# Performance work log

Measured on AMD Instinct MI355X. Metric: run time of the kernel, lower is better.

Reference implementation:

```python
import jax, jax.numpy as jnp
import numpy as np

LN_EPS = 1e-5
DEG_EPS = 1e-6
H = 256
N_VAR = 100000
NUM_CON = 50000
E = 300000


def setup_inputs() -> dict:
    key = jax.random.key(0)
    ks = jax.random.split(key, 8)
    s = 1.0 / np.sqrt(H)
    s2 = 1.0 / np.sqrt(H + 1)
    return {
        "x_var": jax.random.normal(ks[0], (N_VAR, H), dtype=jnp.float32),
        "src": jax.random.randint(ks[1], (E,), 0, N_VAR, dtype=jnp.int32),
        "dst": jax.random.randint(ks[2], (E,), 0, NUM_CON, dtype=jnp.int32),
        "clue_values": jax.random.normal(ks[3], (NUM_CON,), dtype=jnp.float32),
        "num_con": NUM_CON,
        "msg_W": jax.random.uniform(ks[4], (H, H), jnp.float32, -s, s),
        "msg_b": jax.random.uniform(ks[5], (H,), jnp.float32, -s, s),
        "update_W": jax.random.uniform(ks[6], (H, H + 1), jnp.float32, -s2, s2),
        "update_b": jax.random.uniform(ks[7], (H,), jnp.float32, -s2, s2),
        "ln_w": jnp.ones((H,), jnp.float32),
        "ln_b": jnp.zeros((H,), jnp.float32),
    }


def reference(x_var, src, dst, clue_values, num_con, msg_W, msg_b, update_W, update_b, ln_w, ln_b):
    # gather + linear message transform: (E, H)
    msgs = x_var[src] @ msg_W.T + msg_b
    # degree-normalized scatter-add into constraints: (num_con, H)
    agg = jax.ops.segment_sum(msgs, dst, num_segments=num_con)
    deg = jax.ops.segment_sum(jnp.ones((dst.shape[0],), msgs.dtype), dst, num_segments=num_con)
    agg = agg / (deg[:, None] + DEG_EPS)
    # concat clue scalar, update MLP, ReLU
    h = jnp.concatenate([agg, clue_values[:, None]], axis=1)
    out = jax.nn.relu(h @ update_W.T + update_b)
    # LayerNorm over last dim
    mu = out.mean(axis=-1, keepdims=True)
    var = out.var(axis=-1, keepdims=True)
    return (out - mu) * jax.lax.rsqrt(var + LN_EPS) * ln_w + ln_b
```

## Files before the change

### kernel.cpp

```cpp
#include <hip/hip_runtime.h>

#define HD 256
#define LN_EPS 1e-5f
#define DEG_EPS 1e-6f
#define CAP 64
#define C2 264

typedef __attribute__((ext_vector_type(8))) short short8;
typedef __attribute__((ext_vector_type(4))) short s16x4;
typedef __attribute__((ext_vector_type(4))) float f32x4;
typedef __attribute__((ext_vector_type(4))) int i32x4;

__device__ inline unsigned short f2bf(float f) {
    union { float f; unsigned int u; } v; v.f = f;
    unsigned int r = v.u + 0x7FFFu + ((v.u >> 16) & 1u);
    return (unsigned short)(r >> 16);
}
__device__ inline float bf2f(unsigned short h) {
    union { unsigned int u; float f; } v; v.u = ((unsigned int)h) << 16;
    return v.f;
}

__global__ __launch_bounds__(256) void prep0_kernel(
    int* __restrict__ counts, int num_con,
    const float* __restrict__ msg_W, const float* __restrict__ msg_b,
    const float* __restrict__ upd_W,
    unsigned short* __restrict__ w12b, float* __restrict__ bv,
    float* __restrict__ ucol, int zb) {
    int b = blockIdx.x, tid = threadIdx.x;
    if (b < zb) {
        int i = (b * 256 + tid) * 4;
        if (i + 4 <= num_con) *(i32x4*)(counts + i) = (i32x4){0, 0, 0, 0};
        else for (; i < num_con; ++i) counts[i] = 0;
    } else {
        int j = b - zb, k = tid;
        float a0 = 0.f, a1 = 0.f, a2 = 0.f, a3 = 0.f, accb = 0.f;
#pragma unroll 2
        for (int m = 0; m < 256; m += 4) {
            float w0 = upd_W[j * 257 + m + 0];
            float w1 = upd_W[j * 257 + m + 1];
            float w2 = upd_W[j * 257 + m + 2];
            float w3 = upd_W[j * 257 + m + 3];
            a0 = fmaf(w0, msg_W[(m + 0) * 256 + k], a0);
            a1 = fmaf(w1, msg_W[(m + 1) * 256 + k], a1);
            a2 = fmaf(w2, msg_W[(m + 2) * 256 + k], a2);
            a3 = fmaf(w3, msg_W[(m + 3) * 256 + k], a3);
            accb = fmaf(w0, msg_b[m + 0], accb);
            accb = fmaf(w1, msg_b[m + 1], accb);
            accb = fmaf(w2, msg_b[m + 2], accb);
            accb = fmaf(w3, msg_b[m + 3], accb);
        }
        w12b[j * 256 + k] = f2bf((a0 + a1) + (a2 + a3));
        if (k == 0) { bv[j] = accb; ucol[j] = upd_W[j * 257 + 256]; }
    }
}

__global__ __launch_bounds__(256) void xcast_kernel(
    const float* __restrict__ x, unsigned short* __restrict__ xb, long n) {
    long stride = (long)gridDim.x * 256;
    long t0 = (long)blockIdx.x * 256 + threadIdx.x;
#pragma unroll 1
    for (long i = t0 * 8; i + 8 <= n; i += stride * 8) {
        float4 u0 = *(const float4*)(x + i);
        float4 u1 = *(const float4*)(x + i + 4);
        short8 o;
        o[0] = (short)f2bf(u0.x); o[1] = (short)f2bf(u0.y);
        o[2] = (short)f2bf(u0.z); o[3] = (short)f2bf(u0.w);
        o[4] = (short)f2bf(u1.x); o[5] = (short)f2bf(u1.y);
        o[6] = (short)f2bf(u1.z); o[7] = (short)f2bf(u1.w);
        *(short8*)(xb + i) = o;
    }
    if (t0 == 0) for (long i = n & ~7L; i < n; ++i) xb[i] = f2bf(x[i]);
}

__global__ __launch_bounds__(256) void fill_kernel(
    const int* __restrict__ src, const int* __restrict__ dst,
    int* __restrict__ counts, int* __restrict__ eidx, int E) {
    int e = blockIdx.x * 256 + threadIdx.x;
    if (e >= E) return;
    int d = dst[e];
    int p = atomicAdd(&counts[d], 1);
    if (p < CAP) eidx[d * CAP + p] = src[e];
}

__global__ __launch_bounds__(256) void gather_kernel(
    const unsigned short* __restrict__ xb, const int* __restrict__ counts,
    const int* __restrict__ eidx, unsigned short* __restrict__ agg,
    int num_con) {
    int wv   = threadIdx.x >> 6;
    int lane = threadIdx.x & 63;
#pragma unroll 1
    for (int r = 0; r < 4; ++r) {
        int row = blockIdx.x * 16 + wv * 4 + r;
        if (row >= num_con) continue;
        int cnt = counts[row];
        int cgo = min(cnt, CAP);
        int sid = (lane < cgo) ? eidx[row * CAP + lane] : 0;
        float a0 = 0.f, a1 = 0.f, a2 = 0.f, a3 = 0.f;
#pragma unroll 1
        for (int i = 0; i < cgo; i += 8) {
            int s[8];
#pragma unroll
            for (int u = 0; u < 8; ++u) s[u] = __shfl(sid, i + u, 64);
            s16x4 v[8];
#pragma unroll
            for (int u = 0; u < 8; ++u)
                v[u] = *(const s16x4*)(xb + (long)s[u] * HD + lane * 4);
#pragma unroll
            for (int u = 0; u < 8; ++u) {
                float wg = (i + u < cgo) ? 1.f : 0.f;
                a0 = fmaf(bf2f((unsigned short)v[u][0]), wg, a0);
                a1 = fmaf(bf2f((unsigned short)v[u][1]), wg, a1);
                a2 = fmaf(bf2f((unsigned short)v[u][2]), wg, a2);
                a3 = fmaf(bf2f((unsigned short)v[u][3]), wg, a3);
            }
        }
        float sc = 1.0f / ((float)cnt + DEG_EPS);
        s16x4 o;
        o[0] = (short)f2bf(a0 * sc); o[1] = (short)f2bf(a1 * sc);
        o[2] = (short)f2bf(a2 * sc); o[3] = (short)f2bf(a3 * sc);
        *(s16x4*)(agg + (long)row * HD + lane * 4) = o;
    }
}

__global__ __launch_bounds__(256) void gfinal_kernel(
    const unsigned short* __restrict__ agg, const int* __restrict__ counts,
    const float* __restrict__ clue,
    const unsigned short* __restrict__ w12b, const float* __restrict__ bv,
    const float* __restrict__ ucol, const float* __restrict__ upd_b,
    const float* __restrict__ ln_w, const float* __restrict__ ln_b,
    float* __restrict__ out, int num_con, int ntiles) {

    __shared__ unsigned short sA[16 * 256];
    __shared__ float sZ[2][16 * C2];
    const int tid = threadIdx.x, w = tid >> 6, lane = tid & 63;
    const int lr = lane & 15, lg = lane >> 4;

    short8 bfr[4][8];
#pragma unroll
    for (int jt = 0; jt < 4; ++jt)
#pragma unroll
        for (int ks = 0; ks < 8; ++ks)
            bfr[jt][ks] = *(const short8*)(w12b + (w * 64 + jt * 16 + lr) * HD + lg * 8 + ks * 32);
    float uc[4], b2[4], bvv[4];
#pragma unroll
    for (int jt = 0; jt < 4; ++jt) {
        uc[jt]  = ucol[w * 64 + jt * 16 + lr];
        b2[jt]  = upd_b[w * 64 + jt * 16 + lr];
        bvv[jt] = bv[w * 64 + jt * 16 + lr];
    }
    const int seg = tid & 15;
    f32x4 lw[4], lb[4];
#pragma unroll
    for (int k = 0; k < 4; ++k) {
        lw[k] = *(const f32x4*)(ln_w + seg * 16 + k * 4);
        lb[k] = *(const f32x4*)(ln_b + seg * 16 + k * 4);
    }
    const int srow = tid >> 4, scol = (tid & 15) * 16;

    int buf = 0;
#pragma unroll 1
    for (int rt = blockIdx.x; rt < ntiles; rt += gridDim.x) {
        int r0 = rt * 16;
        {
            int arc = min(r0 + srow, num_con - 1);
            const unsigned short* gp = agg + (long)arc * HD + scol;
            short8 v0 = *(const short8*)(gp);
            short8 v1 = *(const short8*)(gp + 8);
            int b0 = (srow * 512 + scol * 2) ^ ((srow & 7) << 4);
            int b1 = (srow * 512 + scol * 2 + 16) ^ ((srow & 7) << 4);
            *(short8*)((char*)sA + b0) = v0;
            *(short8*)((char*)sA + b1) = v1;
        }
        __syncthreads();

        short8 af[8];
#pragma unroll
        for (int ks = 0; ks < 8; ++ks) {
            int byte = (lr * 512 + (ks * 32 + lg * 8) * 2) ^ ((lr & 7) << 4);
            af[ks] = *(const short8*)((char*)sA + byte);
        }

        f32x4 acc[4] = {{0.f,0.f,0.f,0.f},{0.f,0.f,0.f,0.f},{0.f,0.f,0.f,0.f},{0.f,0.f,0.f,0.f}};
#pragma unroll
        for (int ks = 0; ks < 8; ++ks)
#pragma unroll
            for (int jt = 0; jt < 4; ++jt)
                acc[jt] = __builtin_amdgcn_mfma_f32_16x16x32_bf16(af[ks], bfr[jt][ks], acc[jt], 0, 0, 0);

        float cl[4], trow[4];
#pragma unroll
        for (int q = 0; q < 4; ++q) {
            int rr = min(r0 + lg * 4 + q, num_con - 1);
            cl[q] = clue[rr];
            float dvq = (float)counts[rr];
            trow[q] = dvq / (dvq + DEG_EPS);
        }
#pragma unroll
        for (int jt = 0; jt < 4; ++jt)
#pragma unroll
            for (int q = 0; q < 4; ++q) {
                float z = fmaxf(acc[jt][q] + trow[q] * bvv[jt] + uc[jt] * cl[q] + b2[jt], 0.0f);
                sZ[buf][(lg * 4 + q) * C2 + w * 64 + jt * 16 + lr] = z;
            }
        __syncthreads();
        {
            int row = tid >> 4;
            const float* zp = &sZ[buf][row * C2 + seg * 16];
            f32x4 z4[4];
            float s = 0.f, s2 = 0.f;
#pragma unroll
            for (int k = 0; k < 4; ++k) {
                z4[k] = *(const f32x4*)(zp + k * 4);
#pragma unroll
                for (int e = 0; e < 4; ++e) { s += z4[k][e]; s2 += z4[k][e] * z4[k][e]; }
            }
#pragma unroll
            for (int m = 1; m < 16; m <<= 1) {
                s  += __shfl_xor(s,  m, 64);
                s2 += __shfl_xor(s2, m, 64);
            }
            float mu = s * (1.0f / HD);
            float var = s2 * (1.0f / HD) - mu * mu;
            float rs = rsqrtf(var + LN_EPS);
            int grow = r0 + row;
            if (grow < num_con) {
                float* gp = out + (long)grow * HD + seg * 16;
#pragma unroll
                for (int k = 0; k < 4; ++k) {
                    f32x4 o;
#pragma unroll
                    for (int e = 0; e < 4; ++e)
                        o[e] = (z4[k][e] - mu) * rs * lw[k][e] + lb[k][e];
                    *(f32x4*)(gp + k * 4) = o;
                }
            }
        }
        buf ^= 1;
    }
}

extern "C" void kernel_launch(void* const* d_in, const int* in_sizes, int n_in,
                              void* d_out, int out_size, void* d_ws, size_t ws_size,
                              hipStream_t stream) {
    const float* x_var = (const float*)d_in[0];
    const int*   src   = (const int*)d_in[1];
    const int*   dst   = (const int*)d_in[2];
    const float* clue  = (const float*)d_in[3];
    const float* msg_W = (const float*)d_in[5];
    const float* msg_b = (const float*)d_in[6];
    const float* upd_W = (const float*)d_in[7];
    const float* upd_b = (const float*)d_in[8];
    const float* ln_w  = (const float*)d_in[9];
    const float* ln_b  = (const float*)d_in[10];

    int E = in_sizes[1];
    long n_x = in_sizes[0];
    int n_var = (int)(n_x / HD);
    int num_con = out_size / HD;
    int ntiles = (num_con + 15) / 16;

    char* ws = (char*)d_ws;
    int* counts = (int*)ws;
    int* eidx   = (int*)(ws + (((size_t)num_con * 4 + 255) & ~(size_t)255));
    char* after = (char*)(eidx + (size_t)num_con * CAP);
    size_t xoff = ((size_t)(after - ws) + 255) & ~(size_t)255;
    unsigned short* xb = (unsigned short*)(ws + xoff);
    size_t aoff = (xoff + (size_t)n_var * HD * 2 + 255) & ~(size_t)255;
    unsigned short* agg = (unsigned short*)(ws + aoff);
    size_t woff = (aoff + (size_t)num_con * HD * 2 + 255) & ~(size_t)255;
    unsigned short* w12b = (unsigned short*)(ws + woff);
    float* bvp  = (float*)(w12b + 256 * 256);
    float* ucol = bvp + 256;

    int zb = (num_con + 1023) / 1024;
    prep0_kernel<<<zb + 256, 256, 0, stream>>>(
        counts, num_con, msg_W, msg_b, upd_W, w12b, bvp, ucol, zb);

    xcast_kernel<<<2048, 256, 0, stream>>>(x_var, xb, n_x);

    fill_kernel<<<(E + 255) / 256, 256, 0, stream>>>(src, dst, counts, eidx, E);

    gather_kernel<<<(num_con + 15) / 16, 256, 0, stream>>>(
        xb, counts, eidx, agg, num_con);

    gfinal_kernel<<<1024, 256, 0, stream>>>(
        agg, counts, clue, w12b, bvp, ucol, upd_b, ln_w, ln_b,
        (float*)d_out, num_con, ntiles);
}
```

Measured before the change: 128.6 us.

## Apply fused weight before gather and fuse gather with bias, ReLU, LayerNorm

Uses linearity to multiply x_var by the fused message/update weight first, casting to bf16 inside the GEMM, then gathers the transformed rows per constraint. The gather kernel now also applies degree normalization, biases, clue term, ReLU and LayerNorm. This removes the separate cast kernel and the intermediate aggregate buffer round trip. In exchange the GEMM runs over all variable rows instead of the constraint rows, and results are rounded to bf16 before summation.

```diff
diff --git a/kernel.cpp b/kernel.cpp
--- a/kernel.cpp
+++ b/kernel.cpp
@@ -4,7 +4,7 @@
 #define LN_EPS 1e-5f
 #define DEG_EPS 1e-6f
 #define CAP 64
-#define C2 264
+#define CY 264
 
 typedef __attribute__((ext_vector_type(8))) short short8;
 typedef __attribute__((ext_vector_type(4))) short s16x4;
@@ -19,6 +19,14 @@
 __device__ inline float bf2f(unsigned short h) {
     union { unsigned int u; float f; } v; v.u = ((unsigned int)h) << 16;
     return v.f;
+}
+__device__ inline short8 cvt8(float4 u0, float4 u1) {
+    short8 o;
+    o[0] = (short)f2bf(u0.x); o[1] = (short)f2bf(u0.y);
+    o[2] = (short)f2bf(u0.z); o[3] = (short)f2bf(u0.w);
+    o[4] = (short)f2bf(u1.x); o[5] = (short)f2bf(u1.y);
+    o[6] = (short)f2bf(u1.z); o[7] = (short)f2bf(u1.w);
+    return o;
 }
 
 __global__ __launch_bounds__(256) void prep0_kernel(
@@ -55,24 +63,6 @@
     }
 }
 
-__global__ __launch_bounds__(256) void xcast_kernel(
-    const float* __restrict__ x, unsigned short* __restrict__ xb, long n) {
-    long stride = (long)gridDim.x * 256;
-    long t0 = (long)blockIdx.x * 256 + threadIdx.x;
-#pragma unroll 1
-    for (long i = t0 * 8; i + 8 <= n; i += stride * 8) {
-        float4 u0 = *(const float4*)(x + i);
-        float4 u1 = *(const float4*)(x + i + 4);
-        short8 o;
-        o[0] = (short)f2bf(u0.x); o[1] = (short)f2bf(u0.y);
-        o[2] = (short)f2bf(u0.z); o[3] = (short)f2bf(u0.w);
-        o[4] = (short)f2bf(u1.x); o[5] = (short)f2bf(u1.y);
-        o[6] = (short)f2bf(u1.z); o[7] = (short)f2bf(u1.w);
-        *(short8*)(xb + i) = o;
-    }
-    if (t0 == 0) for (long i = n & ~7L; i < n; ++i) xb[i] = f2bf(x[i]);
-}
-
 __global__ __launch_bounds__(256) void fill_kernel(
     const int* __restrict__ src, const int* __restrict__ dst,
     int* __restrict__ counts, int* __restrict__ eidx, int E) {
@@ -83,56 +73,12 @@
     if (p < CAP) eidx[d * CAP + p] = src[e];
 }
 
-__global__ __launch_bounds__(256) void gather_kernel(
-    const unsigned short* __restrict__ xb, const int* __restrict__ counts,
-    const int* __restrict__ eidx, unsigned short* __restrict__ agg,
-    int num_con) {
-    int wv   = threadIdx.x >> 6;
-    int lane = threadIdx.x & 63;
-#pragma unroll 1
-    for (int r = 0; r < 4; ++r) {
-        int row = blockIdx.x * 16 + wv * 4 + r;
-        if (row >= num_con) continue;
-        int cnt = counts[row];
-        int cgo = min(cnt, CAP);
-        int sid = (lane < cgo) ? eidx[row * CAP + lane] : 0;
-        float a0 = 0.f, a1 = 0.f, a2 = 0.f, a3 = 0.f;
-#pragma unroll 1
-        for (int i = 0; i < cgo; i += 8) {
-            int s[8];
-#pragma unroll
-            for (int u = 0; u < 8; ++u) s[u] = __shfl(sid, i + u, 64);
-            s16x4 v[8];
-#pragma unroll
-            for (int u = 0; u < 8; ++u)
-                v[u] = *(const s16x4*)(xb + (long)s[u] * HD + lane * 4);
-#pragma unroll
-            for (int u = 0; u < 8; ++u) {
-                float wg = (i + u < cgo) ? 1.f : 0.f;
-                a0 = fmaf(bf2f((unsigned short)v[u][0]), wg, a0);
-                a1 = fmaf(bf2f((unsigned short)v[u][1]), wg, a1);
-                a2 = fmaf(bf2f((unsigned short)v[u][2]), wg, a2);
-                a3 = fmaf(bf2f((unsigned short)v[u][3]), wg, a3);
-            }
-        }
-        float sc = 1.0f / ((float)cnt + DEG_EPS);
-        s16x4 o;
-        o[0] = (short)f2bf(a0 * sc); o[1] = (short)f2bf(a1 * sc);
-        o[2] = (short)f2bf(a2 * sc); o[3] = (short)f2bf(a3 * sc);
-        *(s16x4*)(agg + (long)row * HD + lane * 4) = o;
-    }
-}
-
-__global__ __launch_bounds__(256) void gfinal_kernel(
-    const unsigned short* __restrict__ agg, const int* __restrict__ counts,
-    const float* __restrict__ clue,
-    const unsigned short* __restrict__ w12b, const float* __restrict__ bv,
-    const float* __restrict__ ucol, const float* __restrict__ upd_b,
-    const float* __restrict__ ln_w, const float* __restrict__ ln_b,
-    float* __restrict__ out, int num_con, int ntiles) {
+__global__ __launch_bounds__(256) void ygemm_kernel(
+    const float* __restrict__ x, const unsigned short* __restrict__ w12b,
+    unsigned short* __restrict__ y, int n_var, int ntiles) {
 
     __shared__ unsigned short sA[16 * 256];
-    __shared__ float sZ[2][16 * C2];
+    __shared__ unsigned short sY[2][16 * CY];
     const int tid = threadIdx.x, w = tid >> 6, lane = tid & 63;
     const int lr = lane & 15, lg = lane >> 4;
 
@@ -142,20 +88,7 @@
 #pragma unroll
         for (int ks = 0; ks < 8; ++ks)
             bfr[jt][ks] = *(const short8*)(w12b + (w * 64 + jt * 16 + lr) * HD + lg * 8 + ks * 32);
-    float uc[4], b2[4], bvv[4];
-#pragma unroll
-    for (int jt = 0; jt < 4; ++jt) {
-        uc[jt]  = ucol[w * 64 + jt * 16 + lr];
-        b2[jt]  = upd_b[w * 64 + jt * 16 + lr];
-        bvv[jt] = bv[w * 64 + jt * 16 + lr];
-    }
-    const int seg = tid & 15;
-    f32x4 lw[4], lb[4];
-#pragma unroll
-    for (int k = 0; k < 4; ++k) {
-        lw[k] = *(const f32x4*)(ln_w + seg * 16 + k * 4);
-        lb[k] = *(const f32x4*)(ln_b + seg * 16 + k * 4);
-    }
+
     const int srow = tid >> 4, scol = (tid & 15) * 16;
 
     int buf = 0;
@@ -163,14 +96,16 @@
     for (int rt = blockIdx.x; rt < ntiles; rt += gridDim.x) {
         int r0 = rt * 16;
         {
-            int arc = min(r0 + srow, num_con - 1);
-            const unsigned short* gp = agg + (long)arc * HD + scol;
-            short8 v0 = *(const short8*)(gp);
-            short8 v1 = *(const short8*)(gp + 8);
+            int arc = min(r0 + srow, n_var - 1);
+            const float* gp = x + (long)arc * HD + scol;
+            float4 u0 = *(const float4*)(gp);
+            float4 u1 = *(const float4*)(gp + 4);
+            float4 u2 = *(const float4*)(gp + 8);
+            float4 u3 = *(const float4*)(gp + 12);
             int b0 = (srow * 512 + scol * 2) ^ ((srow & 7) << 4);
             int b1 = (srow * 512 + scol * 2 + 16) ^ ((srow & 7) << 4);
-            *(short8*)((char*)sA + b0) = v0;
-            *(short8*)((char*)sA + b1) = v1;
+            *(short8*)((char*)sA + b0) = cvt8(u0, u1);
+            *(short8*)((char*)sA + b1) = cvt8(u2, u3);
         }
         __syncthreads();
 
@@ -188,56 +123,94 @@
             for (int jt = 0; jt < 4; ++jt)
                 acc[jt] = __builtin_amdgcn_mfma_f32_16x16x32_bf16(af[ks], bfr[jt][ks], acc[jt], 0, 0, 0);
 
-        float cl[4], trow[4];
-#pragma unroll
-        for (int q = 0; q < 4; ++q) {
-            int rr = min(r0 + lg * 4 + q, num_con - 1);
-            cl[q] = clue[rr];
-            float dvq = (float)counts[rr];
-            trow[q] = dvq / (dvq + DEG_EPS);
-        }
 #pragma unroll
         for (int jt = 0; jt < 4; ++jt)
 #pragma unroll
             for (int q = 0; q < 4; ++q) {
-                float z = fmaxf(acc[jt][q] + trow[q] * bvv[jt] + uc[jt] * cl[q] + b2[jt], 0.0f);
-                sZ[buf][(lg * 4 + q) * C2 + w * 64 + jt * 16 + lr] = z;
+                unsigned short mb = f2bf(acc[jt][q]);
+                int nb = __shfl_xor((int)(unsigned int)mb, 1, 64);
+                if (!(lr & 1)) {
+                    unsigned int pk = (unsigned int)mb | (((unsigned int)nb & 0xFFFFu) << 16);
+                    *(unsigned int*)((char*)&sY[buf][0] +
+                        ((lg * 4 + q) * CY + w * 64 + jt * 16 + lr) * 2) = pk;
+                }
             }
         __syncthreads();
         {
-            int row = tid >> 4;
-            const float* zp = &sZ[buf][row * C2 + seg * 16];
-            f32x4 z4[4];
-            float s = 0.f, s2 = 0.f;
-#pragma unroll
-            for (int k = 0; k < 4; ++k) {
-                z4[k] = *(const f32x4*)(zp + k * 4);
-#pragma unroll
-                for (int e = 0; e < 4; ++e) { s += z4[k][e]; s2 += z4[k][e] * z4[k][e]; }
+            int grow = r0 + srow;
+            if (grow < n_var) {
+                const unsigned short* sp = &sY[buf][srow * CY + scol];
+                short8 v0 = *(const short8*)(sp);
+                short8 v1 = *(const short8*)(sp + 8);
+                unsigned short* gp = y + (long)grow * HD + scol;
+                *(short8*)gp = v0;
+                *(short8*)(gp + 8) = v1;
             }
-#pragma unroll
-            for (int m = 1; m < 16; m <<= 1) {
-                s  += __shfl_xor(s,  m, 64);
-                s2 += __shfl_xor(s2, m, 64);
-            }
-            float mu = s * (1.0f / HD);
-            float var = s2 * (1.0f / HD) - mu * mu;
-            float rs = rsqrtf(var + LN_EPS);
-            int grow = r0 + row;
-            if (grow < num_con) {
-                float* gp = out + (long)grow * HD + seg * 16;
-#pragma unroll
-                for (int k = 0; k < 4; ++k) {
-                    f32x4 o;
-#pragma unroll
-                    for (int e = 0; e < 4; ++e)
-                        o[e] = (z4[k][e] - mu) * rs * lw[k][e] + lb[k][e];
-                    *(f32x4*)(gp + k * 4) = o;
-                }
-            }
         }
         buf ^= 1;
     }
+}
+
+__global__ __launch_bounds__(256) void gatherln_kernel(
+    const unsigned short* __restrict__ y, const int* __restrict__ counts,
+    const int* __restrict__ eidx, const float* __restrict__ clue,
+    const float* __restrict__ bv, const float* __restrict__ ucol,
+    const float* __restrict__ upd_b,
+    const float* __restrict__ ln_w, const float* __restrict__ ln_b,
+    float* __restrict__ out, int num_con) {
+    int row  = blockIdx.x * 4 + (threadIdx.x >> 6);
+    int lane = threadIdx.x & 63;
+    if (row >= num_con) return;
+    int cnt = counts[row];
+    int cgo = min(cnt, CAP);
+    int sid = (lane < cgo) ? eidx[row * CAP + lane] : 0;
+    float a0 = 0.f, a1 = 0.f, a2 = 0.f, a3 = 0.f;
+#pragma unroll 1
+    for (int i = 0; i < cgo; i += 8) {
+        int s[8];
+#pragma unroll
+        for (int u = 0; u < 8; ++u) s[u] = __shfl(sid, i + u, 64);
+        s16x4 v[8];
+#pragma unroll
+        for (int u = 0; u < 8; ++u)
+            v[u] = *(const s16x4*)(y + (long)s[u] * HD + lane * 4);
+#pragma unroll
+        for (int u = 0; u < 8; ++u) {
+            float wg = (i + u < cgo) ? 1.f : 0.f;
+            a0 = fmaf(bf2f((unsigned short)v[u][0]), wg, a0);
+            a1 = fmaf(bf2f((unsigned short)v[u][1]), wg, a1);
+            a2 = fmaf(bf2f((unsigned short)v[u][2]), wg, a2);
+            a3 = fmaf(bf2f((unsigned short)v[u][3]), wg, a3);
+        }
+    }
+    float sc = 1.0f / ((float)cnt + DEG_EPS);
+    float tc = (float)cnt * sc;
+    float cl = clue[row];
+    f32x4 bvv = *(const f32x4*)(bv + lane * 4);
+    f32x4 uc4 = *(const f32x4*)(ucol + lane * 4);
+    f32x4 b24 = *(const f32x4*)(upd_b + lane * 4);
+    float z0 = fmaxf(a0 * sc + tc * bvv[0] + cl * uc4[0] + b24[0], 0.0f);
+    float z1 = fmaxf(a1 * sc + tc * bvv[1] + cl * uc4[1] + b24[1], 0.0f);
+    float z2 = fmaxf(a2 * sc + tc * bvv[2] + cl * uc4[2] + b24[2], 0.0f);
+    float z3 = fmaxf(a3 * sc + tc * bvv[3] + cl * uc4[3] + b24[3], 0.0f);
+    float s  = z0 + z1 + z2 + z3;
+    float s2 = z0 * z0 + z1 * z1 + z2 * z2 + z3 * z3;
+#pragma unroll
+    for (int m = 1; m < 64; m <<= 1) {
+        s  += __shfl_xor(s,  m, 64);
+        s2 += __shfl_xor(s2, m, 64);
+    }
+    float mu = s * (1.0f / HD);
+    float var = s2 * (1.0f / HD) - mu * mu;
+    float rs = rsqrtf(var + LN_EPS);
+    f32x4 lw = *(const f32x4*)(ln_w + lane * 4);
+    f32x4 lb = *(const f32x4*)(ln_b + lane * 4);
+    float4 o;
+    o.x = (z0 - mu) * rs * lw[0] + lb[0];
+    o.y = (z1 - mu) * rs * lw[1] + lb[1];
+    o.z = (z2 - mu) * rs * lw[2] + lb[2];
+    o.w = (z3 - mu) * rs * lw[3] + lb[3];
+    *(float4*)(out + (long)row * HD + lane * 4) = o;
 }
 
 extern "C" void kernel_launch(void* const* d_in, const int* in_sizes, int n_in,
@@ -258,17 +231,15 @@
     long n_x = in_sizes[0];
     int n_var = (int)(n_x / HD);
     int num_con = out_size / HD;
-    int ntiles = (num_con + 15) / 16;
+    int ntiles_v = (n_var + 15) / 16;
 
     char* ws = (char*)d_ws;
     int* counts = (int*)ws;
     int* eidx   = (int*)(ws + (((size_t)num_con * 4 + 255) & ~(size_t)255));
     char* after = (char*)(eidx + (size_t)num_con * CAP);
-    size_t xoff = ((size_t)(after - ws) + 255) & ~(size_t)255;
-    unsigned short* xb = (unsigned short*)(ws + xoff);
-    size_t aoff = (xoff + (size_t)n_var * HD * 2 + 255) & ~(size_t)255;
-    unsigned short* agg = (unsigned short*)(ws + aoff);
-    size_t woff = (aoff + (size_t)num_con * HD * 2 + 255) & ~(size_t)255;
+    size_t yoff = ((size_t)(after - ws) + 255) & ~(size_t)255;
+    unsigned short* yv = (unsigned short*)(ws + yoff);
+    size_t woff = (yoff + (size_t)n_var * HD * 2 + 255) & ~(size_t)255;
     unsigned short* w12b = (unsigned short*)(ws + woff);
     float* bvp  = (float*)(w12b + 256 * 256);
     float* ucol = bvp + 256;
@@ -277,14 +248,11 @@
     prep0_kernel<<<zb + 256, 256, 0, stream>>>(
         counts, num_con, msg_W, msg_b, upd_W, w12b, bvp, ucol, zb);
 
-    xcast_kernel<<<2048, 256, 0, stream>>>(x_var, xb, n_x);
-
     fill_kernel<<<(E + 255) / 256, 256, 0, stream>>>(src, dst, counts, eidx, E);
 
-    gather_kernel<<<(num_con + 15) / 16, 256, 0, stream>>>(
-        xb, counts, eidx, agg, num_con);
-
-    gfinal_kernel<<<1024, 256, 0, stream>>>(
-        agg, counts, clue, w12b, bvp, ucol, upd_b, ln_w, ln_b,
-        (float*)d_out, num_con, ntiles);
-}
+    ygemm_kernel<<<2048, 256, 0, stream>>>(x_var, w12b, yv, n_var, ntiles_v);
+
+    gatherln_kernel<<<(num_con + 3) / 4, 256, 0, stream>>>(
+        yv, counts, eidx, clue, bvp, ucol, upd_b, ln_w, ln_b,
+        (float*)d_out, num_con);
+}
```

After: 121.5 us. 5.6% less time.

## Drop bf16 cast pass of x_var and gather fp32 rows directly

Applied to the files above, without the earlier changes.

Removes the separate kernel that converted the whole variable feature matrix to bf16 and instead gathers fp32 rows straight from x_var in the aggregation kernel. The gather is restructured to one constraint row per wave with a 4-way unrolled load loop. This avoids a full read-and-write pass over x_var and one launch, at the cost of doubling bytes per gathered row and lower memory-level parallelism per wave.

```diff
diff --git a/kernel.cpp b/kernel.cpp
--- a/kernel.cpp
+++ b/kernel.cpp
@@ -15,10 +15,6 @@
     union { float f; unsigned int u; } v; v.f = f;
     unsigned int r = v.u + 0x7FFFu + ((v.u >> 16) & 1u);
     return (unsigned short)(r >> 16);
-}
-__device__ inline float bf2f(unsigned short h) {
-    union { unsigned int u; float f; } v; v.u = ((unsigned int)h) << 16;
-    return v.f;
 }
 
 __global__ __launch_bounds__(256) void prep0_kernel(
@@ -55,24 +51,6 @@
     }
 }
 
-__global__ __launch_bounds__(256) void xcast_kernel(
-    const float* __restrict__ x, unsigned short* __restrict__ xb, long n) {
-    long stride = (long)gridDim.x * 256;
-    long t0 = (long)blockIdx.x * 256 + threadIdx.x;
-#pragma unroll 1
-    for (long i = t0 * 8; i + 8 <= n; i += stride * 8) {
-        float4 u0 = *(const float4*)(x + i);
-        float4 u1 = *(const float4*)(x + i + 4);
-        short8 o;
-        o[0] = (short)f2bf(u0.x); o[1] = (short)f2bf(u0.y);
-        o[2] = (short)f2bf(u0.z); o[3] = (short)f2bf(u0.w);
-        o[4] = (short)f2bf(u1.x); o[5] = (short)f2bf(u1.y);
-        o[6] = (short)f2bf(u1.z); o[7] = (short)f2bf(u1.w);
-        *(short8*)(xb + i) = o;
-    }
-    if (t0 == 0) for (long i = n & ~7L; i < n; ++i) xb[i] = f2bf(x[i]);
-}
-
 __global__ __launch_bounds__(256) void fill_kernel(
     const int* __restrict__ src, const int* __restrict__ dst,
     int* __restrict__ counts, int* __restrict__ eidx, int E) {
@@ -84,43 +62,39 @@
 }
 
 __global__ __launch_bounds__(256) void gather_kernel(
-    const unsigned short* __restrict__ xb, const int* __restrict__ counts,
+    const float* __restrict__ x_var, const int* __restrict__ counts,
     const int* __restrict__ eidx, unsigned short* __restrict__ agg,
     int num_con) {
-    int wv   = threadIdx.x >> 6;
+    int row  = blockIdx.x * 4 + (threadIdx.x >> 6);
     int lane = threadIdx.x & 63;
+    if (row >= num_con) return;
+    int cnt = counts[row];
+    int cgo = min(cnt, CAP);
+    int sid = (lane < cgo) ? eidx[row * CAP + lane] : 0;
+    float a0 = 0.f, a1 = 0.f, a2 = 0.f, a3 = 0.f;
 #pragma unroll 1
-    for (int r = 0; r < 4; ++r) {
-        int row = blockIdx.x * 16 + wv * 4 + r;
-        if (row >= num_con) continue;
-        int cnt = counts[row];
-        int cgo = min(cnt, CAP);
-        int sid = (lane < cgo) ? eidx[row * CAP + lane] : 0;
-        float a0 = 0.f, a1 = 0.f, a2 = 0.f, a3 = 0.f;
-#pragma unroll 1
-        for (int i = 0; i < cgo; i += 8) {
-            int s[8];
-#pragma unroll
-            for (int u = 0; u < 8; ++u) s[u] = __shfl(sid, i + u, 64);
-            s16x4 v[8];
-#pragma unroll
-            for (int u = 0; u < 8; ++u)
-                v[u] = *(const s16x4*)(xb + (long)s[u] * HD + lane * 4);
-#pragma unroll
-            for (int u = 0; u < 8; ++u) {
-                float wg = (i + u < cgo) ? 1.f : 0.f;
-                a0 = fmaf(bf2f((unsigned short)v[u][0]), wg, a0);
-                a1 = fmaf(bf2f((unsigned short)v[u][1]), wg, a1);
-                a2 = fmaf(bf2f((unsigned short)v[u][2]), wg, a2);
-                a3 = fmaf(bf2f((unsigned short)v[u][3]), wg, a3);
-            }
-        }
-        float sc = 1.0f / ((float)cnt + DEG_EPS);
-        s16x4 o;
-        o[0] = (short)f2bf(a0 * sc); o[1] = (short)f2bf(a1 * sc);
-        o[2] = (short)f2bf(a2 * sc); o[3] = (short)f2bf(a3 * sc);
-        *(s16x4*)(agg + (long)row * HD + lane * 4) = o;
-    }
+    for (int i = 0; i < cgo; i += 4) {
+        int s0 = __shfl(sid, i, 64);
+        int s1 = __shfl(sid, i + 1, 64);
+        int s2 = __shfl(sid, i + 2, 64);
+        int s3 = __shfl(sid, i + 3, 64);
+        float4 v0 = *(const float4*)(x_var + (long)s0 * HD + lane * 4);
+        float4 v1 = *(const float4*)(x_var + (long)s1 * HD + lane * 4);
+        float4 v2 = *(const float4*)(x_var + (long)s2 * HD + lane * 4);
+        float4 v3 = *(const float4*)(x_var + (long)s3 * HD + lane * 4);
+        float w1 = (i + 1 < cgo) ? 1.f : 0.f;
+        float w2 = (i + 2 < cgo) ? 1.f : 0.f;
+        float w3 = (i + 3 < cgo) ? 1.f : 0.f;
+        a0 += v0.x + v1.x * w1 + v2.x * w2 + v3.x * w3;
+        a1 += v0.y + v1.y * w1 + v2.y * w2 + v3.y * w3;
+        a2 += v0.z + v1.z * w1 + v2.z * w2 + v3.z * w3;
+        a3 += v0.w + v1.w * w1 + v2.w * w2 + v3.w * w3;
+    }
+    float sc = 1.0f / ((float)cnt + DEG_EPS);
+    s16x4 o;
+    o[0] = (short)f2bf(a0 * sc); o[1] = (short)f2bf(a1 * sc);
+    o[2] = (short)f2bf(a2 * sc); o[3] = (short)f2bf(a3 * sc);
+    *(s16x4*)(agg + (long)row * HD + lane * 4) = o;
 }
 
 __global__ __launch_bounds__(256) void gfinal_kernel(
@@ -255,8 +229,6 @@
     const float* ln_b  = (const float*)d_in[10];
 
     int E = in_sizes[1];
-    long n_x = in_sizes[0];
-    int n_var = (int)(n_x / HD);
     int num_con = out_size / HD;
     int ntiles = (num_con + 15) / 16;
 
@@ -264,9 +236,7 @@
     int* counts = (int*)ws;
     int* eidx   = (int*)(ws + (((size_t)num_con * 4 + 255) & ~(size_t)255));
     char* after = (char*)(eidx + (size_t)num_con * CAP);
-    size_t xoff = ((size_t)(after - ws) + 255) & ~(size_t)255;
-    unsigned short* xb = (unsigned short*)(ws + xoff);
-    size_t aoff = (xoff + (size_t)n_var * HD * 2 + 255) & ~(size_t)255;
+    size_t aoff = ((size_t)(after - ws) + 255) & ~(size_t)255;
     unsigned short* agg = (unsigned short*)(ws + aoff);
     size_t woff = (aoff + (size_t)num_con * HD * 2 + 255) & ~(size_t)255;
     unsigned short* w12b = (unsigned short*)(ws + woff);
@@ -277,12 +247,10 @@
     prep0_kernel<<<zb + 256, 256, 0, stream>>>(
         counts, num_con, msg_W, msg_b, upd_W, w12b, bvp, ucol, zb);
 
-    xcast_kernel<<<2048, 256, 0, stream>>>(x_var, xb, n_x);
-
     fill_kernel<<<(E + 255) / 256, 256, 0, stream>>>(src, dst, counts, eidx, E);
 
-    gather_kernel<<<(num_con + 15) / 16, 256, 0, stream>>>(
-        xb, counts, eidx, agg, num_con);
+    gather_kernel<<<(num_con + 3) / 4, 256, 0, stream>>>(
+        x_var, counts, eidx, agg, num_con);
 
     gfinal_kernel<<<1024, 256, 0, stream>>>(
         agg, counts, clue, w12b, bvp, ucol, upd_b, ln_w, ln_b,
```

After: 126.9 us. No clear change (-1.4%).
